# Optimization experiments

Hardware: AMD Instinct MI355X
Metric: run time of the kernel (lower is better)

Reference implementation:

```python
import jax, jax.numpy as jnp
import numpy as np
import math

N = 50000        # nodes
E = 800000       # edges
FEATS = 64
CLASSES = 16
HIDDEN = 64
DEPTH = 10
DIFF = 0.9
EMB_DIM = 1 + int(math.log2(FEATS))   # 7
ADJ_HID = 4 + EMB_DIM                  # 11


def setup_inputs() -> dict:
    key = jax.random.key(0)
    ks = jax.random.split(key, 12)
    x = jax.random.normal(ks[0], (N, FEATS), dtype=jnp.float32)
    src = jax.random.randint(ks[1], (E,), 0, N, dtype=jnp.int64)
    dst = jax.random.randint(ks[2], (E,), 0, N, dtype=jnp.int64)
    s = 0.05
    W1 = jax.random.normal(ks[3], (2 * FEATS, HIDDEN), jnp.float32) * s
    b1 = jnp.zeros((HIDDEN,), jnp.float32)
    W2 = jax.random.normal(ks[4], (HIDDEN, CLASSES), jnp.float32) * s
    b2 = jnp.zeros((CLASSES,), jnp.float32)
    A1 = jax.random.normal(ks[5], (2 + EMB_DIM, ADJ_HID), jnp.float32) * s
    ab1 = jnp.zeros((ADJ_HID,), jnp.float32)
    A2 = jax.random.normal(ks[6], (ADJ_HID, 1), jnp.float32) * s
    ab2 = jnp.zeros((1,), jnp.float32)
    emb = jax.random.normal(ks[7], (FEATS, EMB_DIM), jnp.float32) * s
    return {"x": x, "src": src, "dst": dst, "W1": W1, "b1": b1,
            "W2": W2, "b2": b2, "A1": A1, "ab1": ab1, "A2": A2,
            "ab2": ab2, "emb": emb}


def reference(x, src, dst, W1, b1, W2, b2, A1, ab1, A2, ab2, emb):
    n, f = x.shape
    # cached symmetric GCN normalization: D^-1/2 A D^-1/2
    deg = jax.ops.segment_sum(jnp.ones((src.shape[0],), x.dtype), dst, num_segments=n)
    inv_sqrt = jnp.where(deg > 0, jax.lax.rsqrt(jnp.maximum(deg, 1e-12)), 0.0)
    norm = inv_sqrt[src] * inv_sqrt[dst]   # [E]

    def conv(z):
        return jax.ops.segment_sum(z[src] * norm[:, None], dst, num_segments=n)

    # first diffusion loop (personalized-pagerank style residual blend)
    h0 = x
    z = x
    for _ in range(DEPTH):
        z = conv(z) * DIFF + (1.0 - DIFF) * h0

    # node x class pair MLP (class-major flatten, matching x.t().reshape(-1,1))
    cls = jnp.repeat(jnp.arange(f), n)                 # [f*n]
    pairs = jnp.concatenate([z.T.reshape(-1, 1),
                             h0.T.reshape(-1, 1),
                             emb[cls]], axis=1)        # [f*n, 2+EMB_DIM]
    u = jax.nn.relu(pairs @ A1 + ab1)
    u = (u @ A2 + ab2) / 2.0                           # [f*n, 1]
    z = u.reshape(f, n).T                              # [n, f]

    # dropout is identity in eval mode
    z = jnp.concatenate([z, h0], axis=1)               # [n, 2f]
    z = jax.nn.relu(z @ W1 + b1)
    z = z @ W2 + b2                                    # [n, classes]

    # second diffusion loop over class logits
    g0 = z
    for _ in range(DEPTH):
        z = conv(z) * DIFF + (1.0 - DIFF) * g0
    return z
```

## Files before the change

### kernel.cpp

```cpp
#include <hip/hip_runtime.h>

#define FEATS    64
#define CLASSES  16
#define EMB_DIM  7
#define ADJ_HID  11
#define DIFF     0.9f

__device__ inline float bf2f(unsigned short u) {
    return __uint_as_float(((unsigned int)u) << 16);
}
__device__ inline unsigned short f2bf(float f) {
    unsigned int u = __float_as_uint(f);
    return (unsigned short)((u + 0x7FFFu + ((u >> 16) & 1u)) >> 16);
}


__global__ __launch_bounds__(256) void k_deg(const int* __restrict__ dst, int* __restrict__ deg, int e) {
    int i = blockIdx.x * 256 + threadIdx.x;
    if (i < e) atomicAdd(&deg[dst[i]], 1);
}

__global__ __launch_bounds__(256) void k_invs(const int* __restrict__ deg, float* __restrict__ invs, int n) {
    int i = blockIdx.x * 256 + threadIdx.x;
    if (i < n) { int d = deg[i]; invs[i] = d > 0 ? rsqrtf((float)d) : 0.f; }
}

__global__ __launch_bounds__(256) void k_scan1(const int* __restrict__ deg, int* __restrict__ rowptr,
                                               int* __restrict__ bsum, int n) {
    __shared__ int s[256];
    int tid = threadIdx.x;
    int i = blockIdx.x * 256 + tid;
    int v = (i < n) ? deg[i] : 0;
    s[tid] = v; __syncthreads();
    for (int ofs = 1; ofs < 256; ofs <<= 1) {
        int t = (tid >= ofs) ? s[tid - ofs] : 0;
        __syncthreads(); s[tid] += t; __syncthreads();
    }
    if (i < n) rowptr[i] = s[tid] - v;
    if (tid == 255) bsum[blockIdx.x] = s[255];
}

__global__ __launch_bounds__(256) void k_scan2(int* __restrict__ bsum, int nb) {
    __shared__ int s[256];
    int tid = threadIdx.x;
    int v = (tid < nb) ? bsum[tid] : 0;
    s[tid] = v; __syncthreads();
    for (int ofs = 1; ofs < 256; ofs <<= 1) {
        int t = (tid >= ofs) ? s[tid - ofs] : 0;
        __syncthreads(); s[tid] += t; __syncthreads();
    }
    if (tid < nb) bsum[tid] = s[tid] - v;
}

__global__ __launch_bounds__(256) void k_scan3(int* __restrict__ rowptr, const int* __restrict__ bsum,
                                               int n, int e) {
    int i = blockIdx.x * 256 + threadIdx.x;
    if (i < n) rowptr[i] += bsum[i >> 8];
    if (i == n) rowptr[n] = e;
}

__global__ __launch_bounds__(256) void k_scatter(const int* __restrict__ src, const int* __restrict__ dst,
                                                 const float* __restrict__ invs, const int* __restrict__ rowptr,
                                                 int* __restrict__ cnt, int2* __restrict__ edge, int e) {
    int i = blockIdx.x * 256 + threadIdx.x;
    if (i >= e) return;
    int d = dst[i], sv = src[i];
    int pos = rowptr[d] + atomicAdd(&cnt[d], 1);
    edge[pos] = make_int2(sv, __float_as_int(invs[sv] * invs[d]));
}


__global__ __launch_bounds__(256) void k_cast(const float4* __restrict__ in, ushort4* __restrict__ out, int total4) {
    int i = blockIdx.x * 256 + threadIdx.x;
    if (i < total4) {
        float4 v = in[i];
        ushort4 o;
        o.x = f2bf(v.x); o.y = f2bf(v.y); o.z = f2bf(v.z); o.w = f2bf(v.w);
        out[i] = o;
    }
}


__global__ __launch_bounds__(256) void k_conv64b(const ushort4* __restrict__ zin, const ushort4* __restrict__ h0b,
                                                 ushort4* __restrict__ zout, const int* __restrict__ rowptr,
                                                 const int2* __restrict__ edge, int n) {
    int wq = (blockIdx.x * 256 + threadIdx.x) >> 6;
    int n0 = wq * 4;
    if (n0 >= n) return;
    int lane = threadIdx.x & 63;
    int g = lane >> 4, c = lane & 15;

    int v = 0;
    if (lane < 5) v = rowptr[min(n0 + lane, n)];
    int r0 = __shfl(v, 0), r1 = __shfl(v, 1), r2 = __shfl(v, 2),
        r3 = __shfl(v, 3), r4 = __shfl(v, 4);

    ushort4 h4 = make_ushort4(0, 0, 0, 0);
    if (n0 + g < n) h4 = h0b[(size_t)(n0 + g) * 16 + c];

    float a[4][4];
    #pragma unroll
    for (int j = 0; j < 4; ++j)
        #pragma unroll
        for (int f = 0; f < 4; ++f) a[j][f] = 0.f;

    for (int eb = r0; eb < r4; eb += 64) {
        int2 pe = edge[min(eb + lane, r4 - 1)];
        int   es = pe.x;
        float ew = __int_as_float(pe.y);
        #pragma unroll
        for (int k = 0; k < 16; ++k) {
            int s   = k * 4 + g;
            int idx = eb + s;
            int   srcn = __shfl(es, s);
            float wraw = __shfl(ew, s);
            float w = (idx < r4) ? wraw : 0.f;
            int nid = (idx >= r1) + (idx >= r2) + (idx >= r3);
            ushort4 vv = zin[(size_t)srcn * 16 + c];
            float f0 = bf2f(vv.x), f1 = bf2f(vv.y), f2 = bf2f(vv.z), f3 = bf2f(vv.w);
            #pragma unroll
            for (int j = 0; j < 4; ++j) {
                float sel = (nid == j) ? w : 0.f;
                a[j][0] = fmaf(sel, f0, a[j][0]);
                a[j][1] = fmaf(sel, f1, a[j][1]);
                a[j][2] = fmaf(sel, f2, a[j][2]);
                a[j][3] = fmaf(sel, f3, a[j][3]);
            }
        }
    }

    #pragma unroll
    for (int j = 0; j < 4; ++j) {
        #pragma unroll
        for (int f = 0; f < 4; ++f) {
            a[j][f] += __shfl_xor(a[j][f], 16);
            a[j][f] += __shfl_xor(a[j][f], 32);
        }
    }

    if (n0 + g < n) {
        float o0 = (g == 0) ? a[0][0] : (g == 1) ? a[1][0] : (g == 2) ? a[2][0] : a[3][0];
        float o1 = (g == 0) ? a[0][1] : (g == 1) ? a[1][1] : (g == 2) ? a[2][1] : a[3][1];
        float o2 = (g == 0) ? a[0][2] : (g == 1) ? a[1][2] : (g == 2) ? a[2][2] : a[3][2];
        float o3 = (g == 0) ? a[0][3] : (g == 1) ? a[1][3] : (g == 2) ? a[2][3] : a[3][3];
        ushort4 o;
        o.x = f2bf(o0 * DIFF + (1.f - DIFF) * bf2f(h4.x));
        o.y = f2bf(o1 * DIFF + (1.f - DIFF) * bf2f(h4.y));
        o.z = f2bf(o2 * DIFF + (1.f - DIFF) * bf2f(h4.z));
        o.w = f2bf(o3 * DIFF + (1.f - DIFF) * bf2f(h4.w));
        zout[(size_t)(n0 + g) * 16 + c] = o;
    }
}


__global__ __launch_bounds__(256) void k_conv16(const float4* __restrict__ zin4, const float4* __restrict__ g04,
                                                float4* __restrict__ zout4, const int* __restrict__ rowptr,
                                                const int2* __restrict__ edge, int n) {
    int wq = (blockIdx.x * 256 + threadIdx.x) >> 6;
    int n0 = wq * 4;
    if (n0 >= n) return;
    int lane = threadIdx.x & 63;
    int g = lane >> 2, c = lane & 3;

    int v = 0;
    if (lane < 5) v = rowptr[min(n0 + lane, n)];
    int r0 = __shfl(v, 0), r1 = __shfl(v, 1), r2 = __shfl(v, 2),
        r3 = __shfl(v, 3), r4 = __shfl(v, 4);

    float4 h = make_float4(0.f, 0.f, 0.f, 0.f);
    if (g < 4 && n0 + g < n) h = g04[(size_t)(n0 + g) * 4 + c];

    float a[4][4];
    #pragma unroll
    for (int j = 0; j < 4; ++j)
        #pragma unroll
        for (int f = 0; f < 4; ++f) a[j][f] = 0.f;

    for (int eb = r0; eb < r4; eb += 64) {
        int2 pe = edge[min(eb + lane, r4 - 1)];
        int   es = pe.x;
        float ew = __int_as_float(pe.y);
        #pragma unroll
        for (int k = 0; k < 4; ++k) {
            int s   = k * 16 + g;
            int idx = eb + s;
            int   srcn = __shfl(es, s);
            float wraw = __shfl(ew, s);
            float w = (idx < r4) ? wraw : 0.f;
            int nid = (idx >= r1) + (idx >= r2) + (idx >= r3);
            float4 vv = zin4[(size_t)srcn * 4 + c];
            #pragma unroll
            for (int j = 0; j < 4; ++j) {
                float sel = (nid == j) ? w : 0.f;
                a[j][0] = fmaf(sel, vv.x, a[j][0]);
                a[j][1] = fmaf(sel, vv.y, a[j][1]);
                a[j][2] = fmaf(sel, vv.z, a[j][2]);
                a[j][3] = fmaf(sel, vv.w, a[j][3]);
            }
        }
    }

    #pragma unroll
    for (int j = 0; j < 4; ++j) {
        #pragma unroll
        for (int f = 0; f < 4; ++f) {
            a[j][f] += __shfl_xor(a[j][f], 4);
            a[j][f] += __shfl_xor(a[j][f], 8);
            a[j][f] += __shfl_xor(a[j][f], 16);
            a[j][f] += __shfl_xor(a[j][f], 32);
        }
    }

    if (g < 4 && n0 + g < n) {
        float o0 = (g == 0) ? a[0][0] : (g == 1) ? a[1][0] : (g == 2) ? a[2][0] : a[3][0];
        float o1 = (g == 0) ? a[0][1] : (g == 1) ? a[1][1] : (g == 2) ? a[2][1] : a[3][1];
        float o2 = (g == 0) ? a[0][2] : (g == 1) ? a[1][2] : (g == 2) ? a[2][2] : a[3][2];
        float o3 = (g == 0) ? a[0][3] : (g == 1) ? a[1][3] : (g == 2) ? a[2][3] : a[3][3];
        float4 o;
        o.x = o0 * DIFF + (1.f - DIFF) * h.x;
        o.y = o1 * DIFF + (1.f - DIFF) * h.y;
        o.z = o2 * DIFF + (1.f - DIFF) * h.z;
        o.w = o3 * DIFF + (1.f - DIFF) * h.w;
        zout4[(size_t)(n0 + g) * 4 + c] = o;
    }
}


#define PM_GRID 768

__global__ __launch_bounds__(256) void k_pairmlp(const unsigned short* __restrict__ z1, const float* __restrict__ x,
                                                 const float* __restrict__ W1, const float* __restrict__ b1,
                                                 const float* __restrict__ W2, const float* __restrict__ b2,
                                                 const float* __restrict__ A1, const float* __restrict__ ab1,
                                                 const float* __restrict__ A2, const float* __restrict__ ab2,
                                                 const float* __restrict__ emb,
                                                 float* __restrict__ g0, int n, int ntiles) {
    __shared__ float W1s[128 * 64];
    __shared__ float W2s[64 * 16];
    __shared__ float in_s[16][128];
    __shared__ float hid[16 * 65];
    __shared__ float eA1T[ADJ_HID * 64];
    __shared__ float a0s[ADJ_HID], a1s[ADJ_HID], a2s[ADJ_HID];
    __shared__ float ab2s;

    int tid = threadIdx.x;
    const ushort4* z4p = (const ushort4*)z1;
    const float4*  x4p = (const float4*)x;

    #pragma unroll
    for (int k = 0; k < 32; ++k) W1s[tid + k * 256] = W1[tid + k * 256];
    #pragma unroll
    for (int k = 0; k < 4; ++k)  W2s[tid + k * 256] = W2[tid + k * 256];
    if (tid < ADJ_HID) { a0s[tid] = A1[tid]; a1s[tid] = A1[ADJ_HID + tid]; a2s[tid] = A2[tid]; }
    if (tid == 0) ab2s = ab2[0];
    for (int idx = tid; idx < ADJ_HID * 64; idx += 256) {
        int h = idx >> 6, c = idx & 63;
        float s = ab1[h];
        #pragma unroll
        for (int j = 0; j < EMB_DIM; j++) s = fmaf(emb[c * EMB_DIM + j], A1[(2 + j) * ADJ_HID + h], s);
        eA1T[idx] = s;
    }
    __syncthreads();

    for (int tile = blockIdx.x; tile < ntiles; tile += PM_GRID) {
        int base = tile * 16;

        {
            int nl = tid >> 4, c4 = tid & 15;
            int node = base + nl; if (node > n - 1) node = n - 1;
            ushort4 z4 = z4p[(size_t)node * 16 + c4];
            float4  x4 = x4p[(size_t)node * 16 + c4];
            float zf0 = bf2f(z4.x), zf1 = bf2f(z4.y), zf2 = bf2f(z4.z), zf3 = bf2f(z4.w);
            float o0 = ab2s, o1 = ab2s, o2 = ab2s, o3 = ab2s;
            #pragma unroll
            for (int h = 0; h < ADJ_HID; h++) {
                float a0 = a0s[h], a1 = a1s[h], a2 = a2s[h];
                float4 ee = *(const float4*)&eA1T[h * 64 + c4 * 4];
                float t;
                t = fmaf(zf0, a0, fmaf(x4.x, a1, ee.x)); t = fmaxf(t, 0.f); o0 = fmaf(t, a2, o0);
                t = fmaf(zf1, a0, fmaf(x4.y, a1, ee.y)); t = fmaxf(t, 0.f); o1 = fmaf(t, a2, o1);
                t = fmaf(zf2, a0, fmaf(x4.z, a1, ee.z)); t = fmaxf(t, 0.f); o2 = fmaf(t, a2, o2);
                t = fmaf(zf3, a0, fmaf(x4.w, a1, ee.w)); t = fmaxf(t, 0.f); o3 = fmaf(t, a2, o3);
            }
            *(float4*)&in_s[nl][c4 * 4]      = make_float4(o0 * 0.5f, o1 * 0.5f, o2 * 0.5f, o3 * 0.5f);
            *(float4*)&in_s[nl][64 + c4 * 4] = x4;
        }
        __syncthreads();

        {
            int lane = tid & 63, wv = tid >> 6;
            int nb0 = wv * 4;
            float bv = b1[lane];
            float acc[4];
            #pragma unroll
            for (int j = 0; j < 4; ++j) acc[j] = bv;
            #pragma unroll 8
            for (int rb = 0; rb < 128; rb += 4) {
                float w0 = W1s[(rb    ) * 64 + lane];
                float w1 = W1s[(rb + 1) * 64 + lane];
                float w2 = W1s[(rb + 2) * 64 + lane];
                float w3 = W1s[(rb + 3) * 64 + lane];
                #pragma unroll
                for (int j = 0; j < 4; ++j) {
                    float4 iv = *(const float4*)&in_s[nb0 + j][rb];
                    acc[j] = fmaf(iv.w, w3, fmaf(iv.z, w2, fmaf(iv.y, w1, fmaf(iv.x, w0, acc[j]))));
                }
            }
            #pragma unroll
            for (int j = 0; j < 4; ++j) hid[(nb0 + j) * 65 + lane] = fmaxf(acc[j], 0.f);
        }
        __syncthreads();

        {
            int c  = tid & 15;
            int nl = tid >> 4;
            float ac = b2[c];
            #pragma unroll
            for (int h = 0; h < 64; ++h)
                ac = fmaf(hid[nl * 65 + h], W2s[h * 16 + c], ac);
            int n0 = base + nl;
            if (n0 < n) g0[(size_t)n0 * 16 + c] = ac;
        }
        __syncthreads();
    }
}


extern "C" void kernel_launch(void* const* d_in, const int* in_sizes, int n_in,
                              void* d_out, int out_size, void* d_ws, size_t ws_size,
                              hipStream_t stream) {
    const float* x   = (const float*)d_in[0];
    const int*   src = (const int*)d_in[1];
    const int*   dst = (const int*)d_in[2];
    const float* W1  = (const float*)d_in[3];
    const float* b1  = (const float*)d_in[4];
    const float* W2  = (const float*)d_in[5];
    const float* b2  = (const float*)d_in[6];
    const float* A1  = (const float*)d_in[7];
    const float* ab1 = (const float*)d_in[8];
    const float* A2  = (const float*)d_in[9];
    const float* ab2 = (const float*)d_in[10];
    const float* emb = (const float*)d_in[11];

    int n = in_sizes[0] / FEATS;
    int e = in_sizes[1];

    char* ws = (char*)d_ws;
    size_t off = 0;
    auto alloc = [&](size_t bytes) {
        void* p = ws + off;
        off += bytes;
        off = (off + 255) & ~(size_t)255;
        return p;
    };

    int*     deg    = (int*)    alloc((size_t)n * 4);
    float*   invs   = (float*)  alloc((size_t)n * 4);
    int*     rowptr = (int*)    alloc((size_t)(n + 1) * 4);
    int*     cnt    = (int*)    alloc((size_t)n * 4);
    int*     bsum   = (int*)    alloc(1024);
    int2*    edge   = (int2*)   alloc((size_t)e * 8 + 256);
    ushort4* xb     = (ushort4*)alloc((size_t)n * 64 * 2);
    ushort4* zbA    = (ushort4*)alloc((size_t)n * 64 * 2);
    ushort4* zbB    = (ushort4*)alloc((size_t)n * 64 * 2);
    float*   g0     = (float*)  alloc((size_t)n * 16 * 4);
    float*   g1     = (float*)  alloc((size_t)n * 16 * 4);
    float*   g2     = (float*)  alloc((size_t)n * 16 * 4);

    hipMemsetAsync(deg, 0, (size_t)n * 4, stream);
    hipMemsetAsync(cnt, 0, (size_t)n * 4, stream);

    int eb = (e + 255) / 256;
    int nb = (n + 255) / 256;

    k_deg    <<<eb, 256, 0, stream>>>(dst, deg, e);
    k_invs   <<<nb, 256, 0, stream>>>(deg, invs, n);
    k_scan1  <<<nb, 256, 0, stream>>>(deg, rowptr, bsum, n);
    k_scan2  <<<1, 256, 0, stream>>>(bsum, nb);
    k_scan3  <<<(n + 256) / 256, 256, 0, stream>>>(rowptr, bsum, n, e);
    k_scatter<<<eb, 256, 0, stream>>>(src, dst, invs, rowptr, cnt, edge, e);

    int total4 = n * 16;
    k_cast<<<(total4 + 255) / 256, 256, 0, stream>>>((const float4*)x, xb, total4);

    int nquad = (n + 3) / 4;
    int cblocks = (nquad + 3) / 4;

    const ushort4* zin = xb;
    ushort4* zout = zbA;
    for (int it = 0; it < 10; ++it) {
        k_conv64b<<<cblocks, 256, 0, stream>>>(zin, xb, zout, rowptr, edge, n);
        zin  = zout;
        zout = (it == 0) ? zbB : ((zout == zbA) ? zbB : zbA);
    }
    const unsigned short* z1 = (const unsigned short*)zin;

    int ntiles = (n + 15) / 16;
    k_pairmlp<<<PM_GRID, 256, 0, stream>>>(z1, x, W1, b1, W2, b2,
                                           A1, ab1, A2, ab2, emb, g0, n, ntiles);

    const float* gin = g0;
    float* gout = g1;
    for (int it = 0; it < 10; ++it) {
        float* out = (it == 9) ? (float*)d_out : gout;
        k_conv16<<<cblocks, 256, 0, stream>>>((const float4*)gin, (const float4*)g0, (float4*)out,
                                              rowptr, edge, n);
        gin  = out;
        gout = (gout == g1) ? g2 : g1;
    }
}
```

Baseline: 626.4 us.

## Pack CSR edges into 32-bit words and partition scatter by destination range

```diff
diff --git a/kernel.cpp b/kernel.cpp
--- a/kernel.cpp
+++ b/kernel.cpp
@@ -1,4 +1,5 @@
 #include <hip/hip_runtime.h>
+#include <hip/hip_fp16.h>
 
 #define FEATS    64
 #define CLASSES  16
@@ -12,6 +13,9 @@
 __device__ inline unsigned short f2bf(float f) {
     unsigned int u = __float_as_uint(f);
     return (unsigned short)((u + 0x7FFFu + ((u >> 16) & 1u)) >> 16);
+}
+__device__ inline float edge_w(unsigned int u) {
+    return __half2float(__ushort_as_half((unsigned short)(u & 0xFFFFu)));
 }
 
 
@@ -61,12 +65,21 @@
 
 __global__ __launch_bounds__(256) void k_scatter(const int* __restrict__ src, const int* __restrict__ dst,
                                                  const float* __restrict__ invs, const int* __restrict__ rowptr,
-                                                 int* __restrict__ cnt, int2* __restrict__ edge, int e) {
-    int i = blockIdx.x * 256 + threadIdx.x;
-    if (i >= e) return;
-    int d = dst[i], sv = src[i];
-    int pos = rowptr[d] + atomicAdd(&cnt[d], 1);
-    edge[pos] = make_int2(sv, __float_as_int(invs[sv] * invs[d]));
+                                                 int* __restrict__ cnt, unsigned int* __restrict__ edge,
+                                                 int e, int n) {
+    int grp = blockIdx.x & 7;
+    int lo = (int)(((long long)n * grp) >> 3);
+    int hi = (int)(((long long)n * (grp + 1)) >> 3);
+    int stride = (gridDim.x >> 3) * 256;
+    for (int i = (blockIdx.x >> 3) * 256 + threadIdx.x; i < e; i += stride) {
+        int d = dst[i];
+        if (d < lo || d >= hi) continue;
+        int sv = src[i];
+        int pos = rowptr[d] + atomicAdd(&cnt[d], 1);
+        float nm = invs[sv] * invs[d];
+        unsigned short hb = __half_as_ushort(__float2half(nm));
+        edge[pos] = ((unsigned int)sv << 16) | (unsigned int)hb;
+    }
 }
 
 
@@ -83,7 +96,7 @@
 
 __global__ __launch_bounds__(256) void k_conv64b(const ushort4* __restrict__ zin, const ushort4* __restrict__ h0b,
                                                  ushort4* __restrict__ zout, const int* __restrict__ rowptr,
-                                                 const int2* __restrict__ edge, int n) {
+                                                 const unsigned int* __restrict__ edge, int n) {
     int wq = (blockIdx.x * 256 + threadIdx.x) >> 6;
     int n0 = wq * 4;
     if (n0 >= n) return;
@@ -105,16 +118,14 @@
         for (int f = 0; f < 4; ++f) a[j][f] = 0.f;
 
     for (int eb = r0; eb < r4; eb += 64) {
-        int2 pe = edge[min(eb + lane, r4 - 1)];
-        int   es = pe.x;
-        float ew = __int_as_float(pe.y);
+        unsigned int pe = edge[min(eb + lane, r4 - 1)];
         #pragma unroll
         for (int k = 0; k < 16; ++k) {
             int s   = k * 4 + g;
             int idx = eb + s;
-            int   srcn = __shfl(es, s);
-            float wraw = __shfl(ew, s);
-            float w = (idx < r4) ? wraw : 0.f;
+            unsigned int ue = __shfl(pe, s);
+            int   srcn = (int)(ue >> 16);
+            float w = (idx < r4) ? edge_w(ue) : 0.f;
             int nid = (idx >= r1) + (idx >= r2) + (idx >= r3);
             ushort4 vv = zin[(size_t)srcn * 16 + c];
             float f0 = bf2f(vv.x), f1 = bf2f(vv.y), f2 = bf2f(vv.z), f3 = bf2f(vv.w);
@@ -155,7 +166,7 @@
 
 __global__ __launch_bounds__(256) void k_conv16(const float4* __restrict__ zin4, const float4* __restrict__ g04,
                                                 float4* __restrict__ zout4, const int* __restrict__ rowptr,
-                                                const int2* __restrict__ edge, int n) {
+                                                const unsigned int* __restrict__ edge, int n) {
     int wq = (blockIdx.x * 256 + threadIdx.x) >> 6;
     int n0 = wq * 4;
     if (n0 >= n) return;
@@ -177,16 +188,14 @@
         for (int f = 0; f < 4; ++f) a[j][f] = 0.f;
 
     for (int eb = r0; eb < r4; eb += 64) {
-        int2 pe = edge[min(eb + lane, r4 - 1)];
-        int   es = pe.x;
-        float ew = __int_as_float(pe.y);
+        unsigned int pe = edge[min(eb + lane, r4 - 1)];
         #pragma unroll
         for (int k = 0; k < 4; ++k) {
             int s   = k * 16 + g;
             int idx = eb + s;
-            int   srcn = __shfl(es, s);
-            float wraw = __shfl(ew, s);
-            float w = (idx < r4) ? wraw : 0.f;
+            unsigned int ue = __shfl(pe, s);
+            int   srcn = (int)(ue >> 16);
+            float w = (idx < r4) ? edge_w(ue) : 0.f;
             int nid = (idx >= r1) + (idx >= r2) + (idx >= r3);
             float4 vv = zin4[(size_t)srcn * 4 + c];
             #pragma unroll
@@ -354,18 +363,18 @@
         return p;
     };
 
-    int*     deg    = (int*)    alloc((size_t)n * 4);
-    float*   invs   = (float*)  alloc((size_t)n * 4);
-    int*     rowptr = (int*)    alloc((size_t)(n + 1) * 4);
-    int*     cnt    = (int*)    alloc((size_t)n * 4);
-    int*     bsum   = (int*)    alloc(1024);
-    int2*    edge   = (int2*)   alloc((size_t)e * 8 + 256);
-    ushort4* xb     = (ushort4*)alloc((size_t)n * 64 * 2);
-    ushort4* zbA    = (ushort4*)alloc((size_t)n * 64 * 2);
-    ushort4* zbB    = (ushort4*)alloc((size_t)n * 64 * 2);
-    float*   g0     = (float*)  alloc((size_t)n * 16 * 4);
-    float*   g1     = (float*)  alloc((size_t)n * 16 * 4);
-    float*   g2     = (float*)  alloc((size_t)n * 16 * 4);
+    int*          deg    = (int*)          alloc((size_t)n * 4);
+    float*        invs   = (float*)        alloc((size_t)n * 4);
+    int*          rowptr = (int*)          alloc((size_t)(n + 1) * 4);
+    int*          cnt    = (int*)          alloc((size_t)n * 4);
+    int*          bsum   = (int*)          alloc(1024);
+    unsigned int* edge   = (unsigned int*) alloc((size_t)e * 4 + 256);
+    ushort4*      xb     = (ushort4*)      alloc((size_t)n * 64 * 2);
+    ushort4*      zbA    = (ushort4*)      alloc((size_t)n * 64 * 2);
+    ushort4*      zbB    = (ushort4*)      alloc((size_t)n * 64 * 2);
+    float*        g0     = (float*)        alloc((size_t)n * 16 * 4);
+    float*        g1     = (float*)        alloc((size_t)n * 16 * 4);
+    float*        g2     = (float*)        alloc((size_t)n * 16 * 4);
 
     hipMemsetAsync(deg, 0, (size_t)n * 4, stream);
     hipMemsetAsync(cnt, 0, (size_t)n * 4, stream);
@@ -378,7 +387,7 @@
     k_scan1  <<<nb, 256, 0, stream>>>(deg, rowptr, bsum, n);
     k_scan2  <<<1, 256, 0, stream>>>(bsum, nb);
     k_scan3  <<<(n + 256) / 256, 256, 0, stream>>>(rowptr, bsum, n, e);
-    k_scatter<<<eb, 256, 0, stream>>>(src, dst, invs, rowptr, cnt, edge, e);
+    k_scatter<<<1024, 256, 0, stream>>>(src, dst, invs, rowptr, cnt, edge, e, n);
 
     int total4 = n * 16;
     k_cast<<<(total4 + 255) / 256, 256, 0, stream>>>((const float4*)x, xb, total4);
```

Measured after the change: 614.4 us. Within noise of the previous version (-1.9%).
